# Performance work log

Measured on AMD Instinct MI355X. Metric: run time of the kernel, lower is better.

The kernel has to match this reference:

```python
import jax, jax.numpy as jnp
import numpy as np

N = 50000      # total atoms/beads across batch
E = 800000     # total edges (avg degree 16)
H = 128        # hidden_channels
R = 50         # num_rbf
NB = 2         # n_interaction blocks
NG = 64        # num graphs in batch
NT = 100       # num atom types
CUT = 5.0      # upper distance cutoff


def setup_inputs() -> dict:
    key = jax.random.key(0)
    ks = jax.random.split(key, 20)
    atom_types = jax.random.randint(ks[0], (N,), 0, NT)
    pos = jax.random.uniform(ks[1], (N, 3), jnp.float32) * 30.0  # box of 30 Angstrom
    edge_index = jax.random.randint(ks[2], (2, E), 0, N)
    batch = jnp.sort(jax.random.randint(ks[3], (N,), 0, NG))

    def g(k, shape, fan_in):
        return jax.random.normal(k, shape, jnp.float32) * (1.0 / fan_in) ** 0.5

    emb = jax.random.normal(ks[4], (NT, H), jnp.float32) * 0.1
    # filter network per block: Linear(R->H) -> tanh -> Linear(H->H)
    fw1 = g(ks[5], (NB, R, H), R)
    fb1 = jnp.zeros((NB, H), jnp.float32)
    fw2 = g(ks[6], (NB, H, H), H)
    fb2 = jnp.zeros((NB, H), jnp.float32)
    # CFConv lin1 (no bias), lin2 (bias)
    lin1_w = g(ks[7], (NB, H, H), H)
    lin2_w = g(ks[8], (NB, H, H), H)
    lin2_b = jnp.zeros((NB, H), jnp.float32)
    # InteractionBlock output linear
    blk_w = g(ks[9], (NB, H, H), H)
    blk_b = jnp.zeros((NB, H), jnp.float32)
    # output network: Linear(H->H/2) -> tanh -> Linear(H/2->1)
    out_w1 = g(ks[10], (H, H // 2), H)
    out_b1 = jnp.zeros((H // 2,), jnp.float32)
    out_w2 = g(ks[11], (H // 2, 1), H // 2)
    out_b2 = jnp.zeros((1,), jnp.float32)
    return dict(atom_types=atom_types, pos=pos, edge_index=edge_index, batch=batch,
                emb=emb, fw1=fw1, fb1=fb1, fw2=fw2, fb2=fb2,
                lin1_w=lin1_w, lin2_w=lin2_w, lin2_b=lin2_b,
                blk_w=blk_w, blk_b=blk_b,
                out_w1=out_w1, out_b1=out_b1, out_w2=out_w2, out_b2=out_b2)


def reference(atom_types, pos, edge_index, batch, emb, fw1, fb1, fw2, fb2,
              lin1_w, lin2_w, lin2_b, blk_w, blk_b,
              out_w1, out_b1, out_w2, out_b2):
    src, dst = edge_index[0], edge_index[1]
    # pairwise distances along edges (eps keeps sqrt grad finite at coincident points)
    diff = pos[src] - pos[dst]                                  # [E,3]
    d = jnp.sqrt(jnp.sum(diff * diff, axis=-1) + 1e-12)         # [E]
    # Gaussian RBF expansion
    offsets = jnp.linspace(0.0, CUT, R)
    coeff = -0.5 / (offsets[1] - offsets[0]) ** 2
    rbf = jnp.exp(coeff * (d[:, None] - offsets) ** 2)          # [E,R]
    # cosine cutoff envelope
    Cenv = jnp.where(d < CUT, 0.5 * (jnp.cos(d * jnp.pi / CUT) + 1.0), 0.0)  # [E]

    x = emb[atom_types]                                          # [N,H]
    for i in range(NB):
        # filter generation from expanded distances
        W = jnp.tanh(rbf @ fw1[i] + fb1[i]) @ fw2[i] + fb2[i]    # [E,H]
        W = W * Cenv[:, None]
        # CFConv: lin1 -> gather*filter -> scatter-sum -> lin2
        h = x @ lin1_w[i]                                        # [N,H]
        msg = h[src] * W                                         # [E,H]
        agg = jax.ops.segment_sum(msg, dst, num_segments=N)      # [N,H]
        h = agg @ lin2_w[i] + lin2_b[i]
        # InteractionBlock: activation -> lin, residual add in SchNet.forward
        h = jnp.tanh(h)
        x = x + (h @ blk_w[i] + blk_b[i])
    # output network -> per-atom energy, scatter-sum per graph
    e = jnp.tanh(x @ out_w1 + out_b1) @ out_w2 + out_b2          # [N,1]
    energy = jax.ops.segment_sum(e, batch, num_segments=NG)      # [NG,1]
    return energy.flatten()
```

## Files before the change

kernel.cpp:

```cpp
#include <hip/hip_runtime.h>
#include <hip/hip_bf16.h>
#include <math.h>

#define H 128
#define RBF 50
#define CUTF 5.0f
#define PIF 3.14159265358979323846f
#define QT 1024
#define SEG 16

__global__ __launch_bounds__(256) void prep_kernel(
    const float* __restrict__ pos, float4* __restrict__ pos4, int Nn,
    int4* __restrict__ zbase, int zquads,
    const float* __restrict__ fw1, const float* __restrict__ fb1,
    const float* __restrict__ fw2, const float* __restrict__ fb2,
    const float* __restrict__ lin2b, const float* __restrict__ blkw,
    const float* __restrict__ blkb, const float* __restrict__ emb,
    const float* __restrict__ ow1, const float* __restrict__ ob1,
    const float* __restrict__ ow2, const float* __restrict__ ob2,
    float* __restrict__ tab, float* __restrict__ cvec,
    float* __restrict__ e_type, int NT,
    int ZFB, int PB, int FB)
{
    int b = blockIdx.x;
    const int tid = threadIdx.x;
    const int lane = tid & 63;

    if (b < ZFB) {
        int i = b * 256 + tid;
        if (i < zquads) zbase[i] = make_int4(0, 0, 0, 0);
        return;
    }
    b -= ZFB;
    if (b < PB) {
        int n = b * 256 + tid;
        if (n < Nn)
            pos4[n] = make_float4(pos[3 * n], pos[3 * n + 1], pos[3 * n + 2], 0.0f);
        return;
    }
    b -= PB;
    const int h0 = lane, h1 = lane + 64;
    if (b < FB) {
        const int wid = b * 4 + (tid >> 6);
        const int ntab = 2 * (QT + 1);
        if (wid >= ntab + 2) return;
        if (wid >= ntab) {
            const int blk = wid - ntab;
            const float* bwp = blkw + (size_t)blk * H * H;
            float t0 = tanhf(lin2b[blk * H + h0]);
            float t1 = tanhf(lin2b[blk * H + h1]);
            float a0 = blkb[blk * H + h0], a1 = blkb[blk * H + h1];
            #pragma unroll 8
            for (int k = 0; k < 64; ++k) {
                float bb2 = __shfl(t0, k, 64);
                a0 = fmaf(bb2, bwp[k * H + h0], a0);
                a1 = fmaf(bb2, bwp[k * H + h1], a1);
            }
            #pragma unroll 8
            for (int k = 0; k < 64; ++k) {
                float bb2 = __shfl(t1, k, 64);
                a0 = fmaf(bb2, bwp[(64 + k) * H + h0], a0);
                a1 = fmaf(bb2, bwp[(64 + k) * H + h1], a1);
            }
            cvec[blk * H + h0] = a0;
            cvec[blk * H + h1] = a1;
            return;
        }
        const int blk = wid / (QT + 1);
        const int q = wid - blk * (QT + 1);
        const float d = (float)q * (CUTF / (float)QT);
        const float* f1 = fw1 + (size_t)blk * RBF * H;
        const float* f2 = fw2 + (size_t)blk * H * H;
        const float step  = CUTF / 49.0f;
        const float coeff = -0.5f / (step * step);
        float cenv = (d < CUTF) ? 0.5f * (cosf(d * (PIF / CUTF)) + 1.0f) : 0.0f;

        float t0 = fb1[blk * H + h0], t1 = fb1[blk * H + h1];
        #pragma unroll
        for (int r = 0; r < RBF; ++r) {
            float u = d - (float)r * step;
            float rb = expf(coeff * u * u);
            t0 = fmaf(rb, f1[r * H + h0], t0);
            t1 = fmaf(rb, f1[r * H + h1], t1);
        }
        t0 = tanhf(t0); t1 = tanhf(t1);
        float w0 = fb2[blk * H + h0], w1v = fb2[blk * H + h1];
        #pragma unroll 8
        for (int k = 0; k < 64; ++k) {
            float bb2 = __shfl(t0, k, 64);
            w0  = fmaf(bb2, f2[k * H + h0], w0);
            w1v = fmaf(bb2, f2[k * H + h1], w1v);
        }
        #pragma unroll 8
        for (int k = 0; k < 64; ++k) {
            float bb2 = __shfl(t1, k, 64);
            w0  = fmaf(bb2, f2[(64 + k) * H + h0], w0);
            w1v = fmaf(bb2, f2[(64 + k) * H + h1], w1v);
        }
        float* row = tab + ((size_t)blk * (QT + 1) + q) * H;
        row[h0] = w0 * cenv;
        row[h1] = w1v * cenv;
        return;
    }
    b -= FB;
    const int ty = b * 4 + (tid >> 6);
    if (ty >= NT) return;
    float xt0 = emb[(size_t)ty * H + h0];
    float xt1 = emb[(size_t)ty * H + h1];
    #pragma unroll
    for (int blk = 0; blk < 2; ++blk) {
        const float* bwp = blkw + (size_t)blk * H * H;
        float t0 = tanhf(lin2b[blk * H + h0]);
        float t1 = tanhf(lin2b[blk * H + h1]);
        float a0 = blkb[blk * H + h0], a1 = blkb[blk * H + h1];
        #pragma unroll 8
        for (int k = 0; k < 64; ++k) {
            float bb2 = __shfl(t0, k, 64);
            a0 = fmaf(bb2, bwp[k * H + h0], a0);
            a1 = fmaf(bb2, bwp[k * H + h1], a1);
        }
        #pragma unroll 8
        for (int k = 0; k < 64; ++k) {
            float bb2 = __shfl(t1, k, 64);
            a0 = fmaf(bb2, bwp[(64 + k) * H + h0], a0);
            a1 = fmaf(bb2, bwp[(64 + k) * H + h1], a1);
        }
        xt0 += a0; xt1 += a1;
    }
    float y = ob1[lane];
    #pragma unroll 8
    for (int k = 0; k < 64; ++k) {
        float bb2 = __shfl(xt0, k, 64);
        y = fmaf(bb2, ow1[k * 64 + lane], y);
    }
    #pragma unroll 8
    for (int k = 0; k < 64; ++k) {
        float bb2 = __shfl(xt1, k, 64);
        y = fmaf(bb2, ow1[(64 + k) * 64 + lane], y);
    }
    y = tanhf(y) * ow2[lane];
    #pragma unroll
    for (int off = 32; off; off >>= 1) y += __shfl_xor(y, off, 64);
    if (lane == 0) e_type[ty] = y + ob2[0];
}

__global__ __launch_bounds__(256) void edge_prep_kernel(
    const float4* __restrict__ pos4, const int* __restrict__ ei, int E, int CAP,
    int* __restrict__ seg_cnt, int* __restrict__ asrc, int* __restrict__ adst,
    float* __restrict__ ad, int* __restrict__ is_src, int* __restrict__ is_dst)
{
    __shared__ int wtot[4], wbase[4];
    const int tid = threadIdx.x;
    const int lane = tid & 63;
    const int wv = tid >> 6;
    const int gtid = blockIdx.x * 256 + tid;

    int s[4], t[4];
    float d[4];
    bool act[4] = {false, false, false, false};

    const int e0 = gtid * 4;
    if (e0 + 3 < E && (E & 3) == 0) {
        const int4 sv = *(const int4*)(ei + e0);
        const int4 tv = *(const int4*)(ei + E + e0);
        s[0] = sv.x; s[1] = sv.y; s[2] = sv.z; s[3] = sv.w;
        t[0] = tv.x; t[1] = tv.y; t[2] = tv.z; t[3] = tv.w;
        #pragma unroll
        for (int j = 0; j < 4; ++j) {
            float4 ps = pos4[s[j]], pt = pos4[t[j]];
            float dx = ps.x - pt.x, dy = ps.y - pt.y, dz = ps.z - pt.z;
            d[j] = sqrtf(dx * dx + dy * dy + dz * dz + 1e-12f);
            act[j] = (d[j] < CUTF);
        }
    } else if (e0 < E) {
        #pragma unroll
        for (int j = 0; j < 4; ++j) {
            int e = e0 + j;
            if (e < E) {
                s[j] = ei[e]; t[j] = ei[E + e];
                float4 ps = pos4[s[j]], pt = pos4[t[j]];
                float dx = ps.x - pt.x, dy = ps.y - pt.y, dz = ps.z - pt.z;
                d[j] = sqrtf(dx * dx + dy * dy + dz * dz + 1e-12f);
                act[j] = (d[j] < CUTF);
            }
        }
    }

    unsigned long long b[4];
    int mytot = 0;
    #pragma unroll
    for (int j = 0; j < 4; ++j) {
        b[j] = __ballot(act[j]);
        mytot += (int)__popcll(b[j]);
    }
    if (lane == 0) wtot[wv] = mytot;
    __syncthreads();
    if (tid == 0) {
        int t0 = wtot[0], t1 = wtot[1], t2 = wtot[2], t3 = wtot[3];
        int tot = t0 + t1 + t2 + t3;
        int base = 0;
        if (tot) base = atomicAdd(&seg_cnt[blockIdx.x & (SEG - 1)], tot);
        wbase[0] = base; wbase[1] = base + t0;
        wbase[2] = base + t0 + t1; wbase[3] = base + t0 + t1 + t2;
    }
    __syncthreads();

    int run = wbase[wv];
    const int segoff = (int)(blockIdx.x & (SEG - 1)) * CAP;
    const unsigned long long ltm = ((unsigned long long)1 << lane) - 1;
    #pragma unroll
    for (int j = 0; j < 4; ++j) {
        if (act[j]) {
            int p = segoff + run + (int)__popcll(b[j] & ltm);
            asrc[p] = s[j]; adst[p] = t[j]; ad[p] = d[j];
            is_src[s[j]] = 1; is_dst[t[j]] = 1;
        }
        run += (int)__popcll(b[j]);
    }
}

__global__ __launch_bounds__(256) void compact_atoms_kernel(
    const int* __restrict__ is_src, const int* __restrict__ is_dst, int Nn,
    int* __restrict__ cnt4,
    int* __restrict__ src_list, int* __restrict__ dst_list, int* __restrict__ sn_list)
{
    __shared__ int wtot[3][4], wbase[3][4];
    const int tid = threadIdx.x;
    const int lane = tid & 63;
    const int wv = tid >> 6;
    int n = blockIdx.x * 256 + tid;
    bool v[3] = {false, false, false};
    if (n < Nn) {
        v[0] = is_src[n] != 0;
        v[1] = is_dst[n] != 0;
        v[2] = v[0] && !v[1];
    }
    unsigned long long b[3];
    #pragma unroll
    for (int l = 0; l < 3; ++l) {
        b[l] = __ballot(v[l]);
        if (lane == 0) wtot[l][wv] = (int)__popcll(b[l]);
    }
    __syncthreads();
    if (tid == 0) {
        #pragma unroll
        for (int l = 0; l < 3; ++l) {
            int t0 = wtot[l][0], t1 = wtot[l][1], t2 = wtot[l][2], t3 = wtot[l][3];
            int tot = t0 + t1 + t2 + t3;
            int base = 0;
            if (tot) base = atomicAdd(cnt4 + 1 + l, tot);
            wbase[l][0] = base; wbase[l][1] = base + t0;
            wbase[l][2] = base + t0 + t1; wbase[l][3] = base + t0 + t1 + t2;
        }
    }
    __syncthreads();
    const unsigned long long ltm = ((unsigned long long)1 << lane) - 1;
    if (v[0]) src_list[wbase[0][wv] + (int)__popcll(b[0] & ltm)] = n;
    if (v[1]) dst_list[wbase[1][wv] + (int)__popcll(b[1] & ltm)] = n;
    if (v[2]) sn_list[wbase[2][wv] + (int)__popcll(b[2] & ltm)] = n;
}

__global__ __launch_bounds__(256) void edge_scatter_kernel(
    const int* __restrict__ seg_cnt,
    const int* __restrict__ asrc, const int* __restrict__ adst,
    const float* __restrict__ ad, const float* __restrict__ tab,
    const float* __restrict__ hbuf, float* __restrict__ agg, int CAP)
{
    __shared__ int sbase[SEG + 1];
    const int tid = threadIdx.x;
    if (tid == 0) {
        int run = 0;
        #pragma unroll
        for (int s2 = 0; s2 < SEG; ++s2) { sbase[s2] = run; run += seg_cnt[s2]; }
        sbase[SEG] = run;
    }
    __syncthreads();

    const int lane = tid & 63;
    const int wid = (blockIdx.x * blockDim.x + tid) >> 6;
    const int nw  = (gridDim.x * blockDim.x) >> 6;
    const int total = sbase[SEG];
    const float scale = (float)QT / CUTF;

    for (int i = wid; i < total; i += nw) {
        int seg = 0;
        #pragma unroll
        for (int s2 = 1; s2 < SEG; ++s2) seg += (i >= sbase[s2]) ? 1 : 0;
        int slot = seg * CAP + (i - sbase[seg]);

        int s = asrc[slot], t = adst[slot];
        float p = ad[slot] * scale;
        int i0 = (int)p;
        if (i0 > QT - 1) i0 = QT - 1;
        float f = p - (float)i0;
        const float* r0 = tab + (size_t)i0 * H;
        float wl = fmaf(f, r0[H + lane] - r0[lane], r0[lane]);
        float wh = fmaf(f, r0[H + 64 + lane] - r0[64 + lane], r0[64 + lane]);
        float m0 = hbuf[(size_t)s * H + lane] * wl;
        float m1 = hbuf[(size_t)s * H + 64 + lane] * wh;
        atomicAdd(agg + (size_t)t * H + lane, m0);
        atomicAdd(agg + (size_t)t * H + 64 + lane, m1);
    }
}

#define GB 512
#define ZB 128
__global__ __launch_bounds__(256) void gemm_rows_zero_kernel(
    const float* __restrict__ A, const int* __restrict__ atype,
    const float* __restrict__ emb, const float* __restrict__ W,
    float* __restrict__ C,
    const int* __restrict__ rows, const int* __restrict__ cntp,
    float* __restrict__ zbuf, const int* __restrict__ zrows,
    const int* __restrict__ zcntp)
{
    __shared__ float As[32][36];
    __shared__ float Ws[32][128];
    __shared__ int rlist[32], tlist[32];

    const int tid = threadIdx.x;

    if (blockIdx.x >= GB) {
        int zcnt = *zcntp;
        int total = zcnt * 32;
        for (int idx = (blockIdx.x - GB) * 256 + tid; idx < total; idx += ZB * 256) {
            int row = idx >> 5, c = (idx & 31) << 2;
            int r = zrows[row];
            *(float4*)(zbuf + (size_t)r * H + c) = make_float4(0.f, 0.f, 0.f, 0.f);
        }
        return;
    }

    const int cnt = *cntp;
    const int r0 = (tid >> 4) * 2;
    const int c0 = (tid & 15) * 4;

    for (int tile = blockIdx.x; tile * 32 < cnt; tile += GB) {
        __syncthreads();
        if (tid < 32) {
            int idx = tile * 32 + tid;
            int r = (idx < cnt) ? rows[idx] : -1;
            rlist[tid] = r;
            tlist[tid] = (atype && r >= 0) ? atype[r] : 0;
        }
        __syncthreads();

        float acc[2][8];
        #pragma unroll
        for (int j = 0; j < 2; ++j)
            #pragma unroll
            for (int c = 0; c < 8; ++c) acc[j][c] = 0.f;

        for (int kc = 0; kc < H; kc += 32) {
            {
                int lr = tid >> 3;
                int kk = (tid & 7) * 4;
                int r = rlist[lr];
                float4 v = make_float4(0.f, 0.f, 0.f, 0.f);
                if (r >= 0) {
                    const float* base = atype ? (emb + (size_t)tlist[lr] * H)
                                              : (A + (size_t)r * H);
                    v = *(const float4*)(base + kc + kk);
                }
                *(float4*)&As[lr][kk] = v;
            }
            {
                int wr = tid >> 5;
                int wc = (tid & 31) * 4;
                #pragma unroll
                for (int p = 0; p < 4; ++p) {
                    int row = wr + p * 8;
                    *(float4*)&Ws[row][wc] = *(const float4*)(W + (size_t)(kc + row) * H + wc);
                }
            }
            __syncthreads();
            #pragma unroll
            for (int k = 0; k < 32; k += 4) {
                float a_[2][4];
                #pragma unroll
                for (int j = 0; j < 2; ++j)
                    *(float4*)a_[j] = *(const float4*)&As[r0 + j][k];
                #pragma unroll
                for (int kk = 0; kk < 4; ++kk) {
                    float4 wlo = *(const float4*)&Ws[k + kk][c0];
                    float4 whi = *(const float4*)&Ws[k + kk][c0 + 64];
                    float w_[8] = {wlo.x, wlo.y, wlo.z, wlo.w, whi.x, whi.y, whi.z, whi.w};
                    #pragma unroll
                    for (int j = 0; j < 2; ++j)
                        #pragma unroll
                        for (int c = 0; c < 8; ++c)
                            acc[j][c] = fmaf(a_[j][kk], w_[c], acc[j][c]);
                }
            }
            __syncthreads();
        }
        #pragma unroll
        for (int j = 0; j < 2; ++j) {
            int r = rlist[r0 + j];
            if (r < 0) continue;
            #pragma unroll
            for (int hh = 0; hh < 2; ++hh) {
                int cb = c0 + hh * 64;
                *(float4*)(C + (size_t)r * H + cb) = make_float4(
                    acc[j][hh * 4 + 0], acc[j][hh * 4 + 1],
                    acc[j][hh * 4 + 2], acc[j][hh * 4 + 3]);
            }
        }
    }
}

#define UB 512
#define AB 128
__global__ __launch_bounds__(256) void update_x0_kernel(
    const float* __restrict__ agg, const float* __restrict__ l2w,
    const float* __restrict__ l2b, const float* __restrict__ bw,
    const float* __restrict__ bb, float* __restrict__ x,
    const float* __restrict__ emb, const int* __restrict__ atype,
    const int* __restrict__ rows, const int* __restrict__ cntp,
    const int* __restrict__ snrows, const int* __restrict__ sncntp,
    const float* __restrict__ cvec0)
{
    __shared__ float As[32][36];
    __shared__ float Ws[32][128];
    __shared__ float Tl[32][132];
    __shared__ int rlist[32], tlist[32];

    const int tid = threadIdx.x;

    if (blockIdx.x >= UB) {
        int ncnt = *sncntp;
        int total = ncnt * 32;
        for (int idx = (blockIdx.x - UB) * 256 + tid; idx < total; idx += AB * 256) {
            int row = idx >> 5, c = (idx & 31) << 2;
            int r = snrows[row];
            int ty = atype[r];
            float4 ev = *(const float4*)(emb + (size_t)ty * H + c);
            float4 cv = *(const float4*)(cvec0 + c);
            ev.x += cv.x; ev.y += cv.y; ev.z += cv.z; ev.w += cv.w;
            *(float4*)(x + (size_t)r * H + c) = ev;
        }
        return;
    }

    const int cnt = *cntp;
    const int r0 = (tid >> 4) * 2;
    const int c0 = (tid & 15) * 4;

    for (int tile = blockIdx.x; tile * 32 < cnt; tile += UB) {
        __syncthreads();
        if (tid < 32) {
            int idx = tile * 32 + tid;
            int r = (idx < cnt) ? rows[idx] : -1;
            rlist[tid] = r;
            tlist[tid] = (r >= 0) ? atype[r] : 0;
        }
        __syncthreads();

        float acc[2][8];
        #pragma unroll
        for (int j = 0; j < 2; ++j)
            #pragma unroll
            for (int c = 0; c < 8; ++c) acc[j][c] = 0.f;

        for (int kc = 0; kc < H; kc += 32) {
            {
                int lr = tid >> 3;
                int kk = (tid & 7) * 4;
                int r = rlist[lr];
                float4 v = make_float4(0.f, 0.f, 0.f, 0.f);
                if (r >= 0) v = *(const float4*)(agg + (size_t)r * H + kc + kk);
                *(float4*)&As[lr][kk] = v;
            }
            {
                int wr = tid >> 5;
                int wc = (tid & 31) * 4;
                #pragma unroll
                for (int p = 0; p < 4; ++p) {
                    int row = wr + p * 8;
                    *(float4*)&Ws[row][wc] = *(const float4*)(l2w + (size_t)(kc + row) * H + wc);
                }
            }
            __syncthreads();
            #pragma unroll
            for (int k = 0; k < 32; k += 4) {
                float a_[2][4];
                #pragma unroll
                for (int j = 0; j < 2; ++j)
                    *(float4*)a_[j] = *(const float4*)&As[r0 + j][k];
                #pragma unroll
                for (int kk = 0; kk < 4; ++kk) {
                    float4 wlo = *(const float4*)&Ws[k + kk][c0];
                    float4 whi = *(const float4*)&Ws[k + kk][c0 + 64];
                    float w_[8] = {wlo.x, wlo.y, wlo.z, wlo.w, whi.x, whi.y, whi.z, whi.w};
                    #pragma unroll
                    for (int j = 0; j < 2; ++j)
                        #pragma unroll
                        for (int c = 0; c < 8; ++c)
                            acc[j][c] = fmaf(a_[j][kk], w_[c], acc[j][c]);
                }
            }
            __syncthreads();
        }
        #pragma unroll
        for (int j = 0; j < 2; ++j) {
            float4 lo, hi;
            lo.x = tanhf(acc[j][0] + l2b[c0]);      lo.y = tanhf(acc[j][1] + l2b[c0 + 1]);
            lo.z = tanhf(acc[j][2] + l2b[c0 + 2]);  lo.w = tanhf(acc[j][3] + l2b[c0 + 3]);
            hi.x = tanhf(acc[j][4] + l2b[c0 + 64]); hi.y = tanhf(acc[j][5] + l2b[c0 + 65]);
            hi.z = tanhf(acc[j][6] + l2b[c0 + 66]); hi.w = tanhf(acc[j][7] + l2b[c0 + 67]);
            *(float4*)&Tl[r0 + j][c0] = lo;
            *(float4*)&Tl[r0 + j][c0 + 64] = hi;
        }

        float acc2[2][8];
        #pragma unroll
        for (int j = 0; j < 2; ++j)
            #pragma unroll
            for (int c = 0; c < 8; ++c) acc2[j][c] = 0.f;

        for (int kc = 0; kc < H; kc += 32) {
            __syncthreads();
            {
                int wr = tid >> 5;
                int wc = (tid & 31) * 4;
                #pragma unroll
                for (int p = 0; p < 4; ++p) {
                    int row = wr + p * 8;
                    *(float4*)&Ws[row][wc] = *(const float4*)(bw + (size_t)(kc + row) * H + wc);
                }
            }
            __syncthreads();
            #pragma unroll
            for (int k = 0; k < 32; k += 4) {
                float a_[2][4];
                #pragma unroll
                for (int j = 0; j < 2; ++j)
                    *(float4*)a_[j] = *(const float4*)&Tl[r0 + j][kc + k];
                #pragma unroll
                for (int kk = 0; kk < 4; ++kk) {
                    float4 wlo = *(const float4*)&Ws[k + kk][c0];
                    float4 whi = *(const float4*)&Ws[k + kk][c0 + 64];
                    float w_[8] = {wlo.x, wlo.y, wlo.z, wlo.w, whi.x, whi.y, whi.z, whi.w};
                    #pragma unroll
                    for (int j = 0; j < 2; ++j)
                        #pragma unroll
                        for (int c = 0; c < 8; ++c)
                            acc2[j][c] = fmaf(a_[j][kk], w_[c], acc2[j][c]);
                }
            }
        }
        #pragma unroll
        for (int j = 0; j < 2; ++j) {
            int r = rlist[r0 + j];
            if (r < 0) continue;
            int ty = tlist[r0 + j];
            #pragma unroll
            for (int hh = 0; hh < 2; ++hh) {
                int cb = c0 + hh * 64;
                float4 xv = *(const float4*)(emb + (size_t)ty * H + cb);
                xv.x += acc2[j][hh * 4 + 0] + bb[cb];
                xv.y += acc2[j][hh * 4 + 1] + bb[cb + 1];
                xv.z += acc2[j][hh * 4 + 2] + bb[cb + 2];
                xv.w += acc2[j][hh * 4 + 3] + bb[cb + 3];
                *(float4*)(x + (size_t)r * H + cb) = xv;
            }
        }
    }
}

__global__ __launch_bounds__(256) void update_e_kernel(
    const float* __restrict__ agg, const float* __restrict__ l2w,
    const float* __restrict__ l2b, const float* __restrict__ bw,
    const float* __restrict__ bb, const float* __restrict__ x,
    const float* __restrict__ ow1, const float* __restrict__ ob1,
    const float* __restrict__ ow2, const float* __restrict__ ob2,
    float* __restrict__ e_atom,
    const int* __restrict__ rows, const int* __restrict__ cntp)
{
    __shared__ float As[32][36];
    __shared__ float Ws[32][128];
    __shared__ float Tl[32][132];
    __shared__ int rlist[32];

    const int tid = threadIdx.x;
    const int cnt = *cntp;
    const int r0 = (tid >> 4) * 2;
    const int c0 = (tid & 15) * 4;

    for (int tile = blockIdx.x; tile * 32 < cnt; tile += gridDim.x) {
        __syncthreads();
        if (tid < 32) {
            int idx = tile * 32 + tid;
            rlist[tid] = (idx < cnt) ? rows[idx] : -1;
        }
        __syncthreads();

        float acc[2][8];
        #pragma unroll
        for (int j = 0; j < 2; ++j)
            #pragma unroll
            for (int c = 0; c < 8; ++c) acc[j][c] = 0.f;

        for (int kc = 0; kc < H; kc += 32) {
            {
                int lr = tid >> 3;
                int kk = (tid & 7) * 4;
                int r = rlist[lr];
                float4 v = make_float4(0.f, 0.f, 0.f, 0.f);
                if (r >= 0) v = *(const float4*)(agg + (size_t)r * H + kc + kk);
                *(float4*)&As[lr][kk] = v;
            }
            {
                int wr = tid >> 5;
                int wc = (tid & 31) * 4;
                #pragma unroll
                for (int p = 0; p < 4; ++p) {
                    int row = wr + p * 8;
                    *(float4*)&Ws[row][wc] = *(const float4*)(l2w + (size_t)(kc + row) * H + wc);
                }
            }
            __syncthreads();
            #pragma unroll
            for (int k = 0; k < 32; k += 4) {
                float a_[2][4];
                #pragma unroll
                for (int j = 0; j < 2; ++j)
                    *(float4*)a_[j] = *(const float4*)&As[r0 + j][k];
                #pragma unroll
                for (int kk = 0; kk < 4; ++kk) {
                    float4 wlo = *(const float4*)&Ws[k + kk][c0];
                    float4 whi = *(const float4*)&Ws[k + kk][c0 + 64];
                    float w_[8] = {wlo.x, wlo.y, wlo.z, wlo.w, whi.x, whi.y, whi.z, whi.w};
                    #pragma unroll
                    for (int j = 0; j < 2; ++j)
                        #pragma unroll
                        for (int c = 0; c < 8; ++c)
                            acc[j][c] = fmaf(a_[j][kk], w_[c], acc[j][c]);
                }
            }
            __syncthreads();
        }
        #pragma unroll
        for (int j = 0; j < 2; ++j) {
            float4 lo, hi;
            lo.x = tanhf(acc[j][0] + l2b[c0]);      lo.y = tanhf(acc[j][1] + l2b[c0 + 1]);
            lo.z = tanhf(acc[j][2] + l2b[c0 + 2]);  lo.w = tanhf(acc[j][3] + l2b[c0 + 3]);
            hi.x = tanhf(acc[j][4] + l2b[c0 + 64]); hi.y = tanhf(acc[j][5] + l2b[c0 + 65]);
            hi.z = tanhf(acc[j][6] + l2b[c0 + 66]); hi.w = tanhf(acc[j][7] + l2b[c0 + 67]);
            *(float4*)&Tl[r0 + j][c0] = lo;
            *(float4*)&Tl[r0 + j][c0 + 64] = hi;
        }

        float acc2[2][8];
        #pragma unroll
        for (int j = 0; j < 2; ++j)
            #pragma unroll
            for (int c = 0; c < 8; ++c) acc2[j][c] = 0.f;

        for (int kc = 0; kc < H; kc += 32) {
            __syncthreads();
            {
                int wr = tid >> 5;
                int wc = (tid & 31) * 4;
                #pragma unroll
                for (int p = 0; p < 4; ++p) {
                    int row = wr + p * 8;
                    *(float4*)&Ws[row][wc] = *(const float4*)(bw + (size_t)(kc + row) * H + wc);
                }
            }
            __syncthreads();
            #pragma unroll
            for (int k = 0; k < 32; k += 4) {
                float a_[2][4];
                #pragma unroll
                for (int j = 0; j < 2; ++j)
                    *(float4*)a_[j] = *(const float4*)&Tl[r0 + j][kc + k];
                #pragma unroll
                for (int kk = 0; kk < 4; ++kk) {
                    float4 wlo = *(const float4*)&Ws[k + kk][c0];
                    float4 whi = *(const float4*)&Ws[k + kk][c0 + 64];
                    float w_[8] = {wlo.x, wlo.y, wlo.z, wlo.w, whi.x, whi.y, whi.z, whi.w};
                    #pragma unroll
                    for (int j = 0; j < 2; ++j)
                        #pragma unroll
                        for (int c = 0; c < 8; ++c)
                            acc2[j][c] = fmaf(a_[j][kk], w_[c], acc2[j][c]);
                }
            }
        }
        __syncthreads();
        #pragma unroll
        for (int j = 0; j < 2; ++j) {
            int r = rlist[r0 + j];
            #pragma unroll
            for (int hh = 0; hh < 2; ++hh) {
                int cb = c0 + hh * 64;
                float4 xv = make_float4(0.f, 0.f, 0.f, 0.f);
                if (r >= 0) xv = *(const float4*)(x + (size_t)r * H + cb);
                xv.x += acc2[j][hh * 4 + 0] + bb[cb];
                xv.y += acc2[j][hh * 4 + 1] + bb[cb + 1];
                xv.z += acc2[j][hh * 4 + 2] + bb[cb + 2];
                xv.w += acc2[j][hh * 4 + 3] + bb[cb + 3];
                *(float4*)&Tl[r0 + j][cb] = xv;
            }
        }

        float acc3[2][4];
        #pragma unroll
        for (int j = 0; j < 2; ++j)
            #pragma unroll
            for (int c = 0; c < 4; ++c) acc3[j][c] = 0.f;

        for (int kc = 0; kc < H; kc += 32) {
            __syncthreads();
            {
                int wr = tid >> 4;
                int wc = (tid & 15) * 4;
                #pragma unroll
                for (int p = 0; p < 2; ++p) {
                    int row = wr + p * 16;
                    *(float4*)&Ws[row][wc] = *(const float4*)(ow1 + (size_t)(kc + row) * 64 + wc);
                }
            }
            __syncthreads();
            #pragma unroll
            for (int k = 0; k < 32; ++k) {
                float a_[2];
                #pragma unroll
                for (int j = 0; j < 2; ++j) a_[j] = Tl[r0 + j][kc + k];
                float4 wv = *(const float4*)&Ws[k][c0];
                #pragma unroll
                for (int j = 0; j < 2; ++j) {
                    acc3[j][0] = fmaf(a_[j], wv.x, acc3[j][0]);
                    acc3[j][1] = fmaf(a_[j], wv.y, acc3[j][1]);
                    acc3[j][2] = fmaf(a_[j], wv.z, acc3[j][2]);
                    acc3[j][3] = fmaf(a_[j], wv.w, acc3[j][3]);
                }
            }
        }
        const float4 b1v = *(const float4*)(ob1 + c0);
        const float4 w2v = *(const float4*)(ow2 + c0);
        float ep[2];
        #pragma unroll
        for (int j = 0; j < 2; ++j) {
            float v0 = tanhf(acc3[j][0] + b1v.x);
            float v1 = tanhf(acc3[j][1] + b1v.y);
            float v2 = tanhf(acc3[j][2] + b1v.z);
            float v3 = tanhf(acc3[j][3] + b1v.w);
            ep[j] = v0 * w2v.x + v1 * w2v.y + v2 * w2v.z + v3 * w2v.w;
        }
        #pragma unroll
        for (int off = 1; off < 16; off <<= 1) {
            ep[0] += __shfl_xor(ep[0], off, 64);
            ep[1] += __shfl_xor(ep[1], off, 64);
        }
        if ((tid & 15) == 0) {
            const float b2v = ob2[0];
            #pragma unroll
            for (int j = 0; j < 2; ++j) {
                int r = rlist[r0 + j];
                if (r >= 0) e_atom[r] = ep[j] + b2v;
            }
        }
    }
}

__global__ __launch_bounds__(256) void energy_graph_kernel(
    const int* __restrict__ batch, const int* __restrict__ atype,
    const int* __restrict__ is_dst, const float* __restrict__ e_atom,
    const float* __restrict__ e_type, float* __restrict__ energy, int Nn)
{
    const int g = blockIdx.x;
    int lo = 0, hi = Nn;
    while (lo < hi) { int m = (lo + hi) >> 1; if (batch[m] < g) lo = m + 1; else hi = m; }
    const int start = lo;
    hi = Nn;
    while (lo < hi) { int m = (lo + hi) >> 1; if (batch[m] < g + 1) lo = m + 1; else hi = m; }
    const int end = lo;

    float s = 0.0f;
    for (int n = start + (int)threadIdx.x; n < end; n += 256)
        s += is_dst[n] ? e_atom[n] : e_type[atype[n]];
    #pragma unroll
    for (int off = 32; off; off >>= 1) s += __shfl_xor(s, off, 64);
    __shared__ float wp[4];
    if ((threadIdx.x & 63) == 0) wp[threadIdx.x >> 6] = s;
    __syncthreads();
    if (threadIdx.x == 0) energy[g] = wp[0] + wp[1] + wp[2] + wp[3];
}

extern "C" void kernel_launch(void* const* d_in, const int* in_sizes, int n_in,
                              void* d_out, int out_size, void* d_ws, size_t ws_size,
                              hipStream_t stream)
{
    const int*   atype = (const int*)  d_in[0];
    const float* pos   = (const float*)d_in[1];
    const int*   ei    = (const int*)  d_in[2];
    const int*   batch = (const int*)  d_in[3];
    const float* emb   = (const float*)d_in[4];
    const float* fw1   = (const float*)d_in[5];
    const float* fb1   = (const float*)d_in[6];
    const float* fw2   = (const float*)d_in[7];
    const float* fb2   = (const float*)d_in[8];
    const float* lin1w = (const float*)d_in[9];
    const float* lin2w = (const float*)d_in[10];
    const float* lin2b = (const float*)d_in[11];
    const float* blkw  = (const float*)d_in[12];
    const float* blkb  = (const float*)d_in[13];
    const float* ow1   = (const float*)d_in[14];
    const float* ob1   = (const float*)d_in[15];
    const float* ow2   = (const float*)d_in[16];
    const float* ob2   = (const float*)d_in[17];

    const int Nn = in_sizes[0];
    const int E  = in_sizes[2] / 2;
    const int NT = in_sizes[4] / H;
    float* energy = (float*)d_out;

    const int eblocks = (E + 1023) / 1024;
    const int bps = (eblocks + SEG - 1) / SEG;
    const int CAP = bps * 1024;
    const int SEGCAP = SEG * CAP;

    char* w = (char*)d_ws;
    int*   cnt  = (int*)w;
    int*   seg_cnt = cnt + 8;
    int*   is_src = cnt + 32;
    int*   is_dst = is_src + Nn;
    float* x    = (float*)(is_dst + Nn);
    float* hbuf = x + (size_t)Nn * H;
    float* agg  = hbuf + (size_t)Nn * H;
    int*   asrc = (int*)(agg + (size_t)Nn * H);
    int*   adst = asrc + SEGCAP;
    float* ad   = (float*)(adst + SEGCAP);
    int*   src_list = (int*)(ad + SEGCAP);
    int*   dst_list = src_list + Nn;
    int*   sn_list  = dst_list + Nn;
    float* cvec = (float*)(sn_list + Nn);
    float* tab  = cvec + 2 * H;
    float* e_type = tab + 2 * (size_t)(QT + 1) * H;
    float* e_atom = e_type + 128;
    float4* pos4 = (float4*)(e_atom + Nn);

    const int zquads = (128 + 2 * Nn * 4) / 16;
    const int ZFB = (zquads + 255) / 256;
    const int PB  = (Nn + 255) / 256;
    const int FB  = (2 * (QT + 1) + 2 + 3) / 4;
    const int TB  = (NT + 3) / 4;

    prep_kernel<<<ZFB + PB + FB + TB, 256, 0, stream>>>(
        pos, pos4, Nn, (int4*)cnt, zquads,
        fw1, fb1, fw2, fb2, lin2b, blkw, blkb, emb,
        ow1, ob1, ow2, ob2, tab, cvec, e_type, NT, ZFB, PB, FB);

    edge_prep_kernel<<<eblocks, 256, 0, stream>>>(
        pos4, ei, E, CAP, seg_cnt, asrc, adst, ad, is_src, is_dst);
    compact_atoms_kernel<<<(Nn + 255) / 256, 256, 0, stream>>>(
        is_src, is_dst, Nn, cnt, src_list, dst_list, sn_list);

    gemm_rows_zero_kernel<<<GB + ZB, 256, 0, stream>>>(
        nullptr, atype, emb, lin1w, hbuf, src_list, cnt + 1,
        agg, dst_list, cnt + 2);
    edge_scatter_kernel<<<1024, 256, 0, stream>>>(
        seg_cnt, asrc, adst, ad, tab, hbuf, agg, CAP);
    update_x0_kernel<<<UB + AB, 256, 0, stream>>>(
        agg, lin2w, lin2b, blkw, blkb, x, emb, atype,
        dst_list, cnt + 2, sn_list, cnt + 3, cvec);

    gemm_rows_zero_kernel<<<GB + ZB, 256, 0, stream>>>(
        x, nullptr, nullptr, lin1w + (size_t)H * H, hbuf, src_list, cnt + 1,
        agg, dst_list, cnt + 2);
    edge_scatter_kernel<<<1024, 256, 0, stream>>>(
        seg_cnt, asrc, adst, ad, tab + (size_t)(QT + 1) * H, hbuf, agg, CAP);
    update_e_kernel<<<512, 256, 0, stream>>>(
        agg, lin2w + (size_t)H * H, lin2b + H, blkw + (size_t)H * H, blkb + H,
        x, ow1, ob1, ow2, ob2, e_atom, dst_list, cnt + 2);

    energy_graph_kernel<<<out_size, 256, 0, stream>>>(
        batch, atype, is_dst, e_atom, e_type, energy, Nn);
}
```

Before: 235.5 us.

## Precompute per-type lin1 projections and gather by atom type in edge scatter

Block 0's lin1 output depends only on atom type, so a per-type table htype0 is built in the prep kernel and the first per-atom GEMM is removed. For block 1, atoms that are not edge destinations still hold their type-determined x, so a second per-type table htype1 serves them, and only atoms that are both source and destination go through the GEMM. Edge prep stores the source atom type per edge, and zeroing of agg moves into the compaction and update kernels. In exchange there are extra per-edge type loads and an is_dst branch in the second scatter.

```diff
diff --git a/kernel.cpp b/kernel.cpp
--- a/kernel.cpp
+++ b/kernel.cpp
@@ -14,13 +14,15 @@
     int4* __restrict__ zbase, int zquads,
     const float* __restrict__ fw1, const float* __restrict__ fb1,
     const float* __restrict__ fw2, const float* __restrict__ fb2,
-    const float* __restrict__ lin2b, const float* __restrict__ blkw,
-    const float* __restrict__ blkb, const float* __restrict__ emb,
+    const float* __restrict__ lin1w, const float* __restrict__ lin2b,
+    const float* __restrict__ blkw, const float* __restrict__ blkb,
+    const float* __restrict__ emb,
     const float* __restrict__ ow1, const float* __restrict__ ob1,
     const float* __restrict__ ow2, const float* __restrict__ ob2,
     float* __restrict__ tab, float* __restrict__ cvec,
-    float* __restrict__ e_type, int NT,
-    int ZFB, int PB, int FB)
+    float* __restrict__ e_type, float* __restrict__ htype0,
+    float* __restrict__ htype1, int NT,
+    int ZFB, int PB, int FB, int TB, int H0B)
 {
     int b = blockIdx.x;
     const int tid = threadIdx.x;
@@ -103,51 +105,118 @@
         return;
     }
     b -= FB;
-    const int ty = b * 4 + (tid >> 6);
-    if (ty >= NT) return;
-    float xt0 = emb[(size_t)ty * H + h0];
-    float xt1 = emb[(size_t)ty * H + h1];
-    #pragma unroll
-    for (int blk = 0; blk < 2; ++blk) {
-        const float* bwp = blkw + (size_t)blk * H * H;
-        float t0 = tanhf(lin2b[blk * H + h0]);
-        float t1 = tanhf(lin2b[blk * H + h1]);
-        float a0 = blkb[blk * H + h0], a1 = blkb[blk * H + h1];
+    if (b < TB) {
+        const int ty = b * 4 + (tid >> 6);
+        if (ty >= NT) return;
+        float xt0 = emb[(size_t)ty * H + h0];
+        float xt1 = emb[(size_t)ty * H + h1];
+        #pragma unroll
+        for (int blk = 0; blk < 2; ++blk) {
+            const float* bwp = blkw + (size_t)blk * H * H;
+            float t0 = tanhf(lin2b[blk * H + h0]);
+            float t1 = tanhf(lin2b[blk * H + h1]);
+            float a0 = blkb[blk * H + h0], a1 = blkb[blk * H + h1];
+            #pragma unroll 8
+            for (int k = 0; k < 64; ++k) {
+                float bb2 = __shfl(t0, k, 64);
+                a0 = fmaf(bb2, bwp[k * H + h0], a0);
+                a1 = fmaf(bb2, bwp[k * H + h1], a1);
+            }
+            #pragma unroll 8
+            for (int k = 0; k < 64; ++k) {
+                float bb2 = __shfl(t1, k, 64);
+                a0 = fmaf(bb2, bwp[(64 + k) * H + h0], a0);
+                a1 = fmaf(bb2, bwp[(64 + k) * H + h1], a1);
+            }
+            xt0 += a0; xt1 += a1;
+        }
+        float y = ob1[lane];
+        #pragma unroll 8
+        for (int k = 0; k < 64; ++k) {
+            float bb2 = __shfl(xt0, k, 64);
+            y = fmaf(bb2, ow1[k * 64 + lane], y);
+        }
+        #pragma unroll 8
+        for (int k = 0; k < 64; ++k) {
+            float bb2 = __shfl(xt1, k, 64);
+            y = fmaf(bb2, ow1[(64 + k) * 64 + lane], y);
+        }
+        y = tanhf(y) * ow2[lane];
+        #pragma unroll
+        for (int off = 32; off; off >>= 1) y += __shfl_xor(y, off, 64);
+        if (lane == 0) e_type[ty] = y + ob2[0];
+        return;
+    }
+    b -= TB;
+    if (b < H0B) {
+        const int ty = b * 4 + (tid >> 6);
+        if (ty >= NT) return;
+        float x0 = emb[(size_t)ty * H + h0];
+        float x1 = emb[(size_t)ty * H + h1];
+        float a0 = 0.f, a1 = 0.f;
+        #pragma unroll 8
+        for (int k = 0; k < 64; ++k) {
+            float bb2 = __shfl(x0, k, 64);
+            a0 = fmaf(bb2, lin1w[k * H + h0], a0);
+            a1 = fmaf(bb2, lin1w[k * H + h1], a1);
+        }
+        #pragma unroll 8
+        for (int k = 0; k < 64; ++k) {
+            float bb2 = __shfl(x1, k, 64);
+            a0 = fmaf(bb2, lin1w[(64 + k) * H + h0], a0);
+            a1 = fmaf(bb2, lin1w[(64 + k) * H + h1], a1);
+        }
+        htype0[(size_t)ty * H + h0] = a0;
+        htype0[(size_t)ty * H + h1] = a1;
+        return;
+    }
+    b -= H0B;
+    {
+        const int ty = b * 4 + (tid >> 6);
+        if (ty >= NT) return;
+        const float* bwp = blkw;
+        float t0 = tanhf(lin2b[h0]);
+        float t1 = tanhf(lin2b[h1]);
+        float c0 = blkb[h0], c1 = blkb[h1];
         #pragma unroll 8
         for (int k = 0; k < 64; ++k) {
             float bb2 = __shfl(t0, k, 64);
-            a0 = fmaf(bb2, bwp[k * H + h0], a0);
-            a1 = fmaf(bb2, bwp[k * H + h1], a1);
+            c0 = fmaf(bb2, bwp[k * H + h0], c0);
+            c1 = fmaf(bb2, bwp[k * H + h1], c1);
         }
         #pragma unroll 8
         for (int k = 0; k < 64; ++k) {
             float bb2 = __shfl(t1, k, 64);
-            a0 = fmaf(bb2, bwp[(64 + k) * H + h0], a0);
-            a1 = fmaf(bb2, bwp[(64 + k) * H + h1], a1);
-        }
-        xt0 += a0; xt1 += a1;
-    }
-    float y = ob1[lane];
-    #pragma unroll 8
-    for (int k = 0; k < 64; ++k) {
-        float bb2 = __shfl(xt0, k, 64);
-        y = fmaf(bb2, ow1[k * 64 + lane], y);
-    }
-    #pragma unroll 8
-    for (int k = 0; k < 64; ++k) {
-        float bb2 = __shfl(xt1, k, 64);
-        y = fmaf(bb2, ow1[(64 + k) * 64 + lane], y);
-    }
-    y = tanhf(y) * ow2[lane];
-    #pragma unroll
-    for (int off = 32; off; off >>= 1) y += __shfl_xor(y, off, 64);
-    if (lane == 0) e_type[ty] = y + ob2[0];
+            c0 = fmaf(bb2, bwp[(64 + k) * H + h0], c0);
+            c1 = fmaf(bb2, bwp[(64 + k) * H + h1], c1);
+        }
+        float x0 = emb[(size_t)ty * H + h0] + c0;
+        float x1 = emb[(size_t)ty * H + h1] + c1;
+        const float* l1 = lin1w + (size_t)H * H;
+        float a0 = 0.f, a1 = 0.f;
+        #pragma unroll 8
+        for (int k = 0; k < 64; ++k) {
+            float bb2 = __shfl(x0, k, 64);
+            a0 = fmaf(bb2, l1[k * H + h0], a0);
+            a1 = fmaf(bb2, l1[k * H + h1], a1);
+        }
+        #pragma unroll 8
+        for (int k = 0; k < 64; ++k) {
+            float bb2 = __shfl(x1, k, 64);
+            a0 = fmaf(bb2, l1[(64 + k) * H + h0], a0);
+            a1 = fmaf(bb2, l1[(64 + k) * H + h1], a1);
+        }
+        htype1[(size_t)ty * H + h0] = a0;
+        htype1[(size_t)ty * H + h1] = a1;
+    }
 }
 
 __global__ __launch_bounds__(256) void edge_prep_kernel(
-    const float4* __restrict__ pos4, const int* __restrict__ ei, int E, int CAP,
+    const float4* __restrict__ pos4, const int* __restrict__ ei,
+    const int* __restrict__ atype, int E, int CAP,
     int* __restrict__ seg_cnt, int* __restrict__ asrc, int* __restrict__ adst,
-    float* __restrict__ ad, int* __restrict__ is_src, int* __restrict__ is_dst)
+    float* __restrict__ ad, int* __restrict__ asty,
+    int* __restrict__ is_src, int* __restrict__ is_dst)
 {
     __shared__ int wtot[4], wbase[4];
     const int tid = threadIdx.x;
@@ -213,6 +282,7 @@
         if (act[j]) {
             int p = segoff + run + (int)__popcll(b[j] & ltm);
             asrc[p] = s[j]; adst[p] = t[j]; ad[p] = d[j];
+            asty[p] = atype[s[j]];
             is_src[s[j]] = 1; is_dst[t[j]] = 1;
         }
         run += (int)__popcll(b[j]);
@@ -222,29 +292,30 @@
 __global__ __launch_bounds__(256) void compact_atoms_kernel(
     const int* __restrict__ is_src, const int* __restrict__ is_dst, int Nn,
     int* __restrict__ cnt4,
-    int* __restrict__ src_list, int* __restrict__ dst_list, int* __restrict__ sn_list)
+    int* __restrict__ dst_list, int* __restrict__ sd_list,
+    float* __restrict__ agg)
 {
-    __shared__ int wtot[3][4], wbase[3][4];
+    __shared__ int wtot[2][4], wbase[2][4];
     const int tid = threadIdx.x;
     const int lane = tid & 63;
     const int wv = tid >> 6;
     int n = blockIdx.x * 256 + tid;
-    bool v[3] = {false, false, false};
+    bool v[2] = {false, false};
     if (n < Nn) {
-        v[0] = is_src[n] != 0;
-        v[1] = is_dst[n] != 0;
-        v[2] = v[0] && !v[1];
-    }
-    unsigned long long b[3];
+        bool vd = is_dst[n] != 0;
+        v[0] = vd;
+        v[1] = vd && (is_src[n] != 0);
+    }
+    unsigned long long b[2];
     #pragma unroll
-    for (int l = 0; l < 3; ++l) {
+    for (int l = 0; l < 2; ++l) {
         b[l] = __ballot(v[l]);
         if (lane == 0) wtot[l][wv] = (int)__popcll(b[l]);
     }
     __syncthreads();
     if (tid == 0) {
         #pragma unroll
-        for (int l = 0; l < 3; ++l) {
+        for (int l = 0; l < 2; ++l) {
             int t0 = wtot[l][0], t1 = wtot[l][1], t2 = wtot[l][2], t3 = wtot[l][3];
             int tot = t0 + t1 + t2 + t3;
             int base = 0;
@@ -255,16 +326,21 @@
     }
     __syncthreads();
     const unsigned long long ltm = ((unsigned long long)1 << lane) - 1;
-    if (v[0]) src_list[wbase[0][wv] + (int)__popcll(b[0] & ltm)] = n;
-    if (v[1]) dst_list[wbase[1][wv] + (int)__popcll(b[1] & ltm)] = n;
-    if (v[2]) sn_list[wbase[2][wv] + (int)__popcll(b[2] & ltm)] = n;
+    if (v[0]) dst_list[wbase[0][wv] + (int)__popcll(b[0] & ltm)] = n;
+    if (v[1]) sd_list[wbase[1][wv] + (int)__popcll(b[1] & ltm)] = n;
+    if (v[0]) {
+        float4 z = make_float4(0.f, 0.f, 0.f, 0.f);
+        float4* row = (float4*)(agg + (size_t)n * H);
+        #pragma unroll
+        for (int c = 0; c < 32; ++c) row[c] = z;
+    }
 }
 
-__global__ __launch_bounds__(256) void edge_scatter_kernel(
+__global__ __launch_bounds__(256) void edge_scatter0_kernel(
     const int* __restrict__ seg_cnt,
-    const int* __restrict__ asrc, const int* __restrict__ adst,
-    const float* __restrict__ ad, const float* __restrict__ tab,
-    const float* __restrict__ hbuf, float* __restrict__ agg, int CAP)
+    const int* __restrict__ adst, const float* __restrict__ ad,
+    const int* __restrict__ asty, const float* __restrict__ tab,
+    const float* __restrict__ htype0, float* __restrict__ agg, int CAP)
 {
     __shared__ int sbase[SEG + 1];
     const int tid = threadIdx.x;
@@ -288,7 +364,8 @@
         for (int s2 = 1; s2 < SEG; ++s2) seg += (i >= sbase[s2]) ? 1 : 0;
         int slot = seg * CAP + (i - sbase[seg]);
 
-        int s = asrc[slot], t = adst[slot];
+        int t = adst[slot];
+        int ty = asty[slot];
         float p = ad[slot] * scale;
         int i0 = (int)p;
         if (i0 > QT - 1) i0 = QT - 1;
@@ -296,51 +373,77 @@
         const float* r0 = tab + (size_t)i0 * H;
         float wl = fmaf(f, r0[H + lane] - r0[lane], r0[lane]);
         float wh = fmaf(f, r0[H + 64 + lane] - r0[64 + lane], r0[64 + lane]);
-        float m0 = hbuf[(size_t)s * H + lane] * wl;
-        float m1 = hbuf[(size_t)s * H + 64 + lane] * wh;
-        atomicAdd(agg + (size_t)t * H + lane, m0);
-        atomicAdd(agg + (size_t)t * H + 64 + lane, m1);
+        const float* hr = htype0 + (size_t)ty * H;
+        atomicAdd(agg + (size_t)t * H + lane, hr[lane] * wl);
+        atomicAdd(agg + (size_t)t * H + 64 + lane, hr[64 + lane] * wh);
     }
 }
 
-#define GB 512
-#define ZB 128
-__global__ __launch_bounds__(256) void gemm_rows_zero_kernel(
-    const float* __restrict__ A, const int* __restrict__ atype,
-    const float* __restrict__ emb, const float* __restrict__ W,
+__global__ __launch_bounds__(256) void edge_scatter1_kernel(
+    const int* __restrict__ seg_cnt,
+    const int* __restrict__ asrc, const int* __restrict__ adst,
+    const float* __restrict__ ad, const int* __restrict__ asty,
+    const int* __restrict__ is_dst, const float* __restrict__ tab,
+    const float* __restrict__ hbuf, const float* __restrict__ htype1,
+    float* __restrict__ agg, int CAP)
+{
+    __shared__ int sbase[SEG + 1];
+    const int tid = threadIdx.x;
+    if (tid == 0) {
+        int run = 0;
+        #pragma unroll
+        for (int s2 = 0; s2 < SEG; ++s2) { sbase[s2] = run; run += seg_cnt[s2]; }
+        sbase[SEG] = run;
+    }
+    __syncthreads();
+
+    const int lane = tid & 63;
+    const int wid = (blockIdx.x * blockDim.x + tid) >> 6;
+    const int nw  = (gridDim.x * blockDim.x) >> 6;
+    const int total = sbase[SEG];
+    const float scale = (float)QT / CUTF;
+
+    for (int i = wid; i < total; i += nw) {
+        int seg = 0;
+        #pragma unroll
+        for (int s2 = 1; s2 < SEG; ++s2) seg += (i >= sbase[s2]) ? 1 : 0;
+        int slot = seg * CAP + (i - sbase[seg]);
+
+        int s = asrc[slot];
+        int t = adst[slot];
+        float p = ad[slot] * scale;
+        int i0 = (int)p;
+        if (i0 > QT - 1) i0 = QT - 1;
+        float f = p - (float)i0;
+        const float* r0 = tab + (size_t)i0 * H;
+        float wl = fmaf(f, r0[H + lane] - r0[lane], r0[lane]);
+        float wh = fmaf(f, r0[H + 64 + lane] - r0[64 + lane], r0[64 + lane]);
+        const float* hr = is_dst[s] ? (hbuf + (size_t)s * H)
+                                    : (htype1 + (size_t)asty[slot] * H);
+        atomicAdd(agg + (size_t)t * H + lane, hr[lane] * wl);
+        atomicAdd(agg + (size_t)t * H + 64 + lane, hr[64 + lane] * wh);
+    }
+}
+
+__global__ __launch_bounds__(256) void gemm_sd_kernel(
+    const float* __restrict__ A, const float* __restrict__ W,
     float* __restrict__ C,
-    const int* __restrict__ rows, const int* __restrict__ cntp,
-    float* __restrict__ zbuf, const int* __restrict__ zrows,
-    const int* __restrict__ zcntp)
+    const int* __restrict__ rows, const int* __restrict__ cntp)
 {
     __shared__ float As[32][36];
     __shared__ float Ws[32][128];
-    __shared__ int rlist[32], tlist[32];
+    __shared__ int rlist[32];
 
     const int tid = threadIdx.x;
-
-    if (blockIdx.x >= GB) {
-        int zcnt = *zcntp;
-        int total = zcnt * 32;
-        for (int idx = (blockIdx.x - GB) * 256 + tid; idx < total; idx += ZB * 256) {
-            int row = idx >> 5, c = (idx & 31) << 2;
-            int r = zrows[row];
-            *(float4*)(zbuf + (size_t)r * H + c) = make_float4(0.f, 0.f, 0.f, 0.f);
-        }
-        return;
-    }
-
     const int cnt = *cntp;
     const int r0 = (tid >> 4) * 2;
     const int c0 = (tid & 15) * 4;
 
-    for (int tile = blockIdx.x; tile * 32 < cnt; tile += GB) {
+    for (int tile = blockIdx.x; tile * 32 < cnt; tile += gridDim.x) {
         __syncthreads();
         if (tid < 32) {
             int idx = tile * 32 + tid;
-            int r = (idx < cnt) ? rows[idx] : -1;
-            rlist[tid] = r;
-            tlist[tid] = (atype && r >= 0) ? atype[r] : 0;
+            rlist[tid] = (idx < cnt) ? rows[idx] : -1;
         }
         __syncthreads();
 
@@ -356,11 +459,7 @@
                 int kk = (tid & 7) * 4;
                 int r = rlist[lr];
                 float4 v = make_float4(0.f, 0.f, 0.f, 0.f);
-                if (r >= 0) {
-                    const float* base = atype ? (emb + (size_t)tlist[lr] * H)
-                                              : (A + (size_t)r * H);
-                    v = *(const float4*)(base + kc + kk);
-                }
+                if (r >= 0) v = *(const float4*)(A + (size_t)r * H + kc + kk);
                 *(float4*)&As[lr][kk] = v;
             }
             {
@@ -408,16 +507,12 @@
     }
 }
 
-#define UB 512
-#define AB 128
 __global__ __launch_bounds__(256) void update_x0_kernel(
-    const float* __restrict__ agg, const float* __restrict__ l2w,
+    float* __restrict__ agg, const float* __restrict__ l2w,
     const float* __restrict__ l2b, const float* __restrict__ bw,
     const float* __restrict__ bb, float* __restrict__ x,
     const float* __restrict__ emb, const int* __restrict__ atype,
-    const int* __restrict__ rows, const int* __restrict__ cntp,
-    const int* __restrict__ snrows, const int* __restrict__ sncntp,
-    const float* __restrict__ cvec0)
+    const int* __restrict__ rows, const int* __restrict__ cntp)
 {
     __shared__ float As[32][36];
     __shared__ float Ws[32][128];
@@ -425,27 +520,11 @@
     __shared__ int rlist[32], tlist[32];
 
     const int tid = threadIdx.x;
-
-    if (blockIdx.x >= UB) {
-        int ncnt = *sncntp;
-        int total = ncnt * 32;
-        for (int idx = (blockIdx.x - UB) * 256 + tid; idx < total; idx += AB * 256) {
-            int row = idx >> 5, c = (idx & 31) << 2;
-            int r = snrows[row];
-            int ty = atype[r];
-            float4 ev = *(const float4*)(emb + (size_t)ty * H + c);
-            float4 cv = *(const float4*)(cvec0 + c);
-            ev.x += cv.x; ev.y += cv.y; ev.z += cv.z; ev.w += cv.w;
-            *(float4*)(x + (size_t)r * H + c) = ev;
-        }
-        return;
-    }
-
     const int cnt = *cntp;
     const int r0 = (tid >> 4) * 2;
     const int c0 = (tid & 15) * 4;
 
-    for (int tile = blockIdx.x; tile * 32 < cnt; tile += UB) {
+    for (int tile = blockIdx.x; tile * 32 < cnt; tile += gridDim.x) {
         __syncthreads();
         if (tid < 32) {
             int idx = tile * 32 + tid;
@@ -499,6 +578,14 @@
                 }
             }
             __syncthreads();
+        }
+        {
+            float4 z = make_float4(0.f, 0.f, 0.f, 0.f);
+            for (int idx = tid; idx < 32 * 32; idx += 256) {
+                int row = idx >> 5, c = (idx & 31) << 2;
+                int r = rlist[row];
+                if (r >= 0) *(float4*)(agg + (size_t)r * H + c) = z;
+            }
         }
         #pragma unroll
         for (int j = 0; j < 2; ++j) {
@@ -832,13 +919,15 @@
     int*   asrc = (int*)(agg + (size_t)Nn * H);
     int*   adst = asrc + SEGCAP;
     float* ad   = (float*)(adst + SEGCAP);
-    int*   src_list = (int*)(ad + SEGCAP);
-    int*   dst_list = src_list + Nn;
-    int*   sn_list  = dst_list + Nn;
-    float* cvec = (float*)(sn_list + Nn);
+    int*   asty = (int*)(ad + SEGCAP);
+    int*   dst_list = asty + SEGCAP;
+    int*   sd_list  = dst_list + Nn;
+    float* cvec = (float*)(sd_list + Nn);
     float* tab  = cvec + 2 * H;
     float* e_type = tab + 2 * (size_t)(QT + 1) * H;
-    float* e_atom = e_type + 128;
+    float* htype0 = e_type + 128;
+    float* htype1 = htype0 + (size_t)NT * H;
+    float* e_atom = htype1 + (size_t)NT * H;
     float4* pos4 = (float4*)(e_atom + Nn);
 
     const int zquads = (128 + 2 * Nn * 4) / 16;
@@ -846,34 +935,33 @@
     const int PB  = (Nn + 255) / 256;
     const int FB  = (2 * (QT + 1) + 2 + 3) / 4;
     const int TB  = (NT + 3) / 4;
-
-    prep_kernel<<<ZFB + PB + FB + TB, 256, 0, stream>>>(
+    const int H0B = (NT + 3) / 4;
+    const int H1B = (NT + 3) / 4;
+
+    prep_kernel<<<ZFB + PB + FB + TB + H0B + H1B, 256, 0, stream>>>(
         pos, pos4, Nn, (int4*)cnt, zquads,
-        fw1, fb1, fw2, fb2, lin2b, blkw, blkb, emb,
-        ow1, ob1, ow2, ob2, tab, cvec, e_type, NT, ZFB, PB, FB);
+        fw1, fb1, fw2, fb2, lin1w, lin2b, blkw, blkb, emb,
+        ow1, ob1, ow2, ob2, tab, cvec, e_type, htype0, htype1, NT,
+        ZFB, PB, FB, TB, H0B);
 
     edge_prep_kernel<<<eblocks, 256, 0, stream>>>(
-        pos4, ei, E, CAP, seg_cnt, asrc, adst, ad, is_src, is_dst);
+        pos4, ei, atype, E, CAP, seg_cnt, asrc, adst, ad, asty, is_src, is_dst);
     compact_atoms_kernel<<<(Nn + 255) / 256, 256, 0, stream>>>(
-        is_src, is_dst, Nn, cnt, src_list, dst_list, sn_list);
-
-    gemm_rows_zero_kernel<<<GB + ZB, 256, 0, stream>>>(
-        nullptr, atype, emb, lin1w, hbuf, src_list, cnt + 1,
-        agg, dst_list, cnt + 2);
-    edge_scatter_kernel<<<1024, 256, 0, stream>>>(
-        seg_cnt, asrc, adst, ad, tab, hbuf, agg, CAP);
-    update_x0_kernel<<<UB + AB, 256, 0, stream>>>(
-        agg, lin2w, lin2b, blkw, blkb, x, emb, atype,
-        dst_list, cnt + 2, sn_list, cnt + 3, cvec);
-
-    gemm_rows_zero_kernel<<<GB + ZB, 256, 0, stream>>>(
-        x, nullptr, nullptr, lin1w + (size_t)H * H, hbuf, src_list, cnt + 1,
-        agg, dst_list, cnt + 2);
-    edge_scatter_kernel<<<1024, 256, 0, stream>>>(
-        seg_cnt, asrc, adst, ad, tab + (size_t)(QT + 1) * H, hbuf, agg, CAP);
+        is_src, is_dst, Nn, cnt, dst_list, sd_list, agg);
+
+    edge_scatter0_kernel<<<1024, 256, 0, stream>>>(
+        seg_cnt, adst, ad, asty, tab, htype0, agg, CAP);
+    update_x0_kernel<<<512, 256, 0, stream>>>(
+        agg, lin2w, lin2b, blkw, blkb, x, emb, atype, dst_list, cnt + 1);
+
+    gemm_sd_kernel<<<128, 256, 0, stream>>>(
+        x, lin1w + (size_t)H * H, hbuf, sd_list, cnt + 2);
+    edge_scatter1_kernel<<<1024, 256, 0, stream>>>(
+        seg_cnt, asrc, adst, ad, asty, is_dst,
+        tab + (size_t)(QT + 1) * H, hbuf, htype1, agg, CAP);
     update_e_kernel<<<512, 256, 0, stream>>>(
         agg, lin2w + (size_t)H * H, lin2b + H, blkw + (size_t)H * H, blkb + H,
-        x, ow1, ob1, ow2, ob2, e_atom, dst_list, cnt + 2);
+        x, ow1, ob1, ow2, ob2, e_atom, dst_list, cnt + 1);
 
     energy_graph_kernel<<<out_size, 256, 0, stream>>>(
         batch, atype, is_dst, e_atom, e_type, energy, Nn);
```

Result: faster. 223.2 us (-5.3%).
